# Optimization experiments

Hardware: AMD Instinct MI355X
Metric: run time of the kernel (lower is better)

## Reference

```python
import jax, jax.numpy as jnp
import numpy as np

EPS = 1e-8

def rms_norm(x, scale):
    # norm(2,-1)/sqrt(d); x / (rms + eps) * scale
    d = x.shape[-1]
    norm = jnp.sqrt(jnp.sum(x * x, axis=-1, keepdims=True))
    rms = norm / jnp.sqrt(jnp.asarray(d, x.dtype))
    return scale * (x / (rms + EPS))

def setup_inputs() -> dict:
    key = jax.random.key(0)
    B, N, C, FF = 2, 2048, 1024, 4096
    ks = jax.random.split(key, 12)
    s = 0.02
    return {
        "x":  jax.random.normal(ks[0], (B, N, C), jnp.float32),
        "wq": jax.random.normal(ks[1], (C, C), jnp.float32) * s,
        "bq": jnp.zeros((C,), jnp.float32),
        "wk": jax.random.normal(ks[2], (C, C), jnp.float32) * s,
        "bk": jnp.zeros((C,), jnp.float32),
        "wv": jax.random.normal(ks[3], (C, C), jnp.float32) * s,
        "bv": jnp.zeros((C,), jnp.float32),
        "wo": jax.random.normal(ks[4], (C, C), jnp.float32) * s,
        "bo": jnp.zeros((C,), jnp.float32),
        "scale1": jnp.ones((C,), jnp.float32),
        "scale2": jnp.ones((C,), jnp.float32),
        "w1": jax.random.normal(ks[5], (C, FF), jnp.float32) * s,
        "b1": jnp.zeros((FF,), jnp.float32),
        "w2": jax.random.normal(ks[6], (FF, C), jnp.float32) * s,
        "b2": jnp.zeros((C,), jnp.float32),
    }

def reference(x, wq, bq, wk, bk, wv, bv, wo, bo, scale1, scale2, w1, b1, w2, b2):
    B, N, C = x.shape
    H = 16
    D = C // H

    residual = x
    xn = rms_norm(x, scale1)

    def heads(y):  # [B,N,C] -> [B,H,N,D]
        return y.reshape(B, N, H, D).transpose(0, 2, 1, 3)

    q = heads(xn @ wq + bq)
    k = heads(xn @ wk + bk)
    v = heads(xn @ wv + bv)

    # apply_rotary_pos_emb with cos=sin=1: q' = q - roll(q,1,-1), same for k
    q = q - jnp.roll(q, 1, axis=-1)
    k = k - jnp.roll(k, 1, axis=-1)

    # explicit attention (no causal mask in original)
    scores = jnp.einsum('bhnd,bhmd->bhnm', q, k) / jnp.sqrt(jnp.asarray(D, x.dtype))
    probs = jax.nn.softmax(scores, axis=-1)
    attn = jnp.einsum('bhnm,bhmd->bhnd', probs, v)
    attn = attn.transpose(0, 2, 1, 3).reshape(B, N, C)
    attn = attn @ wo + bo

    x = residual + attn
    residual = x
    xn = rms_norm(x, scale2)
    h = jax.nn.gelu(xn @ w1 + b1, approximate=False)  # torch GELU default = exact
    ffn_out = h @ w2 + b2
    return residual + ffn_out
```

## Files before the change

kernel.cpp:

```cpp
#include <hip/hip_runtime.h>
#include <hip/hip_bf16.h>
#include <math.h>

typedef unsigned short u16;
typedef short s16x8 __attribute__((ext_vector_type(8)));
typedef short s16x4 __attribute__((ext_vector_type(4)));
typedef __bf16 bf16x8v __attribute__((ext_vector_type(8)));
typedef float f32x4 __attribute__((ext_vector_type(4)));
typedef unsigned short u16x4 __attribute__((ext_vector_type(4)));

struct Ptr4 { float* p[4]; };
struct TW6 {
    const float* w[6]; u16* o[6]; int mode[6];
    const float *bq, *bk, *bv; float* bqkv;
};

__device__ __forceinline__ u16 f2b(float f) {
    __hip_bfloat16 h = __float2bfloat16(f);
    return __builtin_bit_cast(u16, h);
}

__device__ __forceinline__ float exp2_fast(float x) {
#if __has_builtin(__builtin_amdgcn_exp2f)
    return __builtin_amdgcn_exp2f(x);
#else
    return exp2f(x);
#endif
}

__device__ __forceinline__ f32x4 mfma16(s16x8 a, s16x8 b, f32x4 c) {
    return __builtin_amdgcn_mfma_f32_16x16x32_bf16(
        __builtin_bit_cast(bf16x8v, a), __builtin_bit_cast(bf16x8v, b), c, 0, 0, 0);
}

__device__ __forceinline__ void gl_lds16(const void* g, void* l) {
    typedef const unsigned int __attribute__((address_space(1))) * gp_t;
    typedef unsigned int __attribute__((address_space(3))) * lp_t;
    __builtin_amdgcn_global_load_lds((gp_t)(unsigned long long)g,
                                     (lp_t)(unsigned int)(unsigned long long)l,
                                     16, 0, 0);
}

__device__ __forceinline__ float gelu_fast(float v) {
    float u = 1.5957691216f * (v + 0.044715f * v * v * v);
    return v / (1.f + __expf(-u));
}

#define QSCALE 0.1803368801111244f

__global__ __launch_bounds__(256) void prep_weights(TW6 io) {
    const int z = blockIdx.z, bx = blockIdx.x, by = blockIdx.y;
    const float* W; u16* Wt; int mode = 0, N_, K_, n0, k0;
    if (z < 4) {
        if (bx >= 32) {
            if (z == 0 && bx < 44 && by == 0) {
                const int i = (bx - 32) * 256 + threadIdx.x;
                const int d = i & 1023;
                const int dp = (d & ~63) | ((d + 63) & 63);
                float v;
                if (i < 1024) v = QSCALE * (io.bq[d] - io.bq[dp]);
                else if (i < 2048) v = io.bk[d] - io.bk[dp];
                else v = io.bv[d];
                io.bqkv[i] = v;
            }
            return;
        }
        W = io.w[z]; Wt = io.o[z]; mode = io.mode[z];
        N_ = 1024; K_ = 1024; n0 = bx * 32; k0 = by * 32;
    } else if (z == 4) {
        W = io.w[4]; Wt = io.o[4]; N_ = 4096; K_ = 1024; n0 = bx * 32; k0 = by * 32;
    } else {
        W = io.w[5]; Wt = io.o[5]; N_ = 1024; K_ = 4096; n0 = by * 32; k0 = bx * 32;
    }
    __shared__ u16 tile[32][33];
    const int tx = threadIdx.x & 31, ty = threadIdx.x >> 5;
    const int n = n0 + tx;
    const int np = (n & ~63) | ((n + 63) & 63);
    const float s = (mode == 1) ? QSCALE : 1.f;
#pragma unroll
    for (int i = 0; i < 32; i += 8) {
        const size_t r = (size_t)(k0 + ty + i) * N_;
        float v = W[r + n];
        if (mode) v = (v - W[r + np]) * s;
        tile[ty + i][tx] = f2b(v);
    }
    __syncthreads();
#pragma unroll
    for (int i = 0; i < 32; i += 8)
        Wt[(size_t)(n0 + ty + i) * K_ + k0 + tx] = tile[tx][ty + i];
}

__global__ __launch_bounds__(256) void transpose_v(const u16* __restrict__ qkv,
                                                   u16* __restrict__ vT) {
    __shared__ u16 tile[32][33];
    const int tx = threadIdx.x & 31, ty = threadIdx.x >> 5;
    const int n0 = blockIdx.x * 32, d0 = blockIdx.y * 32, bh = blockIdx.z;
    const int b = bh >> 4, h = bh & 15;
#pragma unroll
    for (int i = 0; i < 32; i += 8)
        tile[ty + i][tx] =
            qkv[(size_t)(b * 2048 + n0 + ty + i) * 3072 + 2048 + h * 64 + d0 + tx];
    __syncthreads();
#pragma unroll
    for (int i = 0; i < 32; i += 8)
        vT[((size_t)bh * 64 + d0 + ty + i) * 2048 + n0 + tx] = tile[tx][ty + i];
}

__global__ __launch_bounds__(256) void rmsnorm_kernel(const float* __restrict__ x,
                                                      const float* __restrict__ scale,
                                                      u16* __restrict__ out) {
    __shared__ float red[4];
    const int t = threadIdx.x, row = blockIdx.x;
    const float4* xr = (const float4*)(x + (size_t)row * 1024);
    float4 v = xr[t];
    float ss = v.x * v.x + v.y * v.y + v.z * v.z + v.w * v.w;
#pragma unroll
    for (int off = 1; off < 64; off <<= 1) ss += __shfl_xor(ss, off);
    if ((t & 63) == 0) red[t >> 6] = ss;
    __syncthreads();
    float tot = red[0] + red[1] + red[2] + red[3];
    float inv = 1.f / (sqrtf(tot * (1.f / 1024.f)) + 1e-8f);
    const float4* sr = (const float4*)scale;
    float4 s = sr[t];
    u16x4 o;
    o[0] = f2b(v.x * inv * s.x);
    o[1] = f2b(v.y * inv * s.y);
    o[2] = f2b(v.z * inv * s.z);
    o[3] = f2b(v.w * inv * s.w);
    ((u16x4*)(out + (size_t)row * 1024))[t] = o;
}

template <int EPI>
__global__ __launch_bounds__(512, 2) void gemm256(const u16* __restrict__ A,
                                                  const u16* __restrict__ Bt,
                                                  const float* __restrict__ bias,
                                                  Ptr4 parts,
                                                  u16* __restrict__ outp,
                                                  int Nout, int nTN, int cpx,
                                                  int Ktot) {
    __shared__ __align__(16) u16 sm[65536];
    u16* As = sm;
    u16* Bs = sm + 32768;

    const int t = threadIdx.x, lane = t & 63, w = t >> 6;
    const int c = lane & 15, qd = lane >> 4;
    const int wm = (w >> 2) * 128, wn = (w & 3) * 64;

    const int id = (int)blockIdx.x;
    const int l = (id & 7) * cpx + (id >> 3);
    const int m0 = (l / nTN) * 256, n0 = (l % nTN) * 256;
    const int k0 = (EPI == 3) ? (int)blockIdx.y * 1024 : 0;
    float* pout = (EPI == 3) ? parts.p[blockIdx.y] : nullptr;

    const int srow = t >> 3;
    const int sch8 = ((t & 7) ^ (srow & 7)) * 8;
    const u16* Ag = A + (size_t)(m0 + srow) * Ktot + k0 + sch8;
    const u16* Bg = Bt + (size_t)(n0 + srow) * Ktot + k0 + sch8;

    float bv[4];
    if (EPI != 3) {
#pragma unroll
        for (int n = 0; n < 4; ++n) bv[n] = bias[n0 + wn + n * 16 + c];
        asm volatile("" ::: "memory");
    }

    auto stageA = [&](int kt, int h, int s) {
        const u16* src = Ag + (size_t)(h * 128) * Ktot + kt * 64;
        u16* dst = As + s * 16384 + h * 8192 + t * 8;
        gl_lds16(src, dst);
        gl_lds16(src + (size_t)64 * Ktot, dst + 4096);
    };
    auto stageB = [&](int kt, int h, int s) {
        const u16* src = Bg + (size_t)(h * 128) * Ktot + kt * 64;
        u16* dst = Bs + s * 16384 + h * 8192 + t * 8;
        gl_lds16(src, dst);
        gl_lds16(src + (size_t)64 * Ktot, dst + 4096);
    };

    stageA(0, 0, 0); stageA(0, 1, 0);
    stageB(0, 0, 0); stageB(0, 1, 0);
    stageB(1, 0, 1); stageB(1, 1, 1);
    asm volatile("s_waitcnt vmcnt(4)" ::: "memory");
    __builtin_amdgcn_s_barrier();
    __builtin_amdgcn_sched_barrier(0);

    f32x4 acc[8][4] = {};

    for (int it = 0; it < 8; ++it) {
        const int ktA = 2 * it, ktB = 2 * it + 1;
        s16x8 bf[4][2];

#pragma unroll
        for (int q = 0; q < 4; ++q) {
            s16x8 af[2][2];
            if (q == 0) {
#pragma unroll
                for (int n = 0; n < 4; ++n)
#pragma unroll
                    for (int ks = 0; ks < 2; ++ks)
                        bf[n][ks] = *(const s16x8*)&Bs[(wn + n * 16 + c) * 64 +
                                                       (((ks * 4 + qd) ^ (c & 7)) * 8)];
            }
#pragma unroll
            for (int mm = 0; mm < 2; ++mm)
#pragma unroll
                for (int ks = 0; ks < 2; ++ks)
                    af[mm][ks] = *(const s16x8*)&As[(wm + (2 * q + mm) * 16 + c) * 64 +
                                                    (((ks * 4 + qd) ^ (c & 7)) * 8)];
            if (q == 0) {
                stageA(ktB, 0, 1);
            } else if (q == 1) {
                stageA(ktB, 1, 1);
                if (ktA + 2 < 16) stageB(ktA + 2, 0, 0);
            } else if (q == 2) {
                if (ktA + 2 < 16) stageB(ktA + 2, 1, 0);
            }
            __builtin_amdgcn_s_barrier();
            asm volatile("s_waitcnt lgkmcnt(0)" ::: "memory");
            __builtin_amdgcn_sched_barrier(0);
            __builtin_amdgcn_s_setprio(1);
#pragma unroll
            for (int mm = 0; mm < 2; ++mm)
#pragma unroll
                for (int n = 0; n < 4; ++n)
#pragma unroll
                    for (int ks = 0; ks < 2; ++ks)
                        acc[2 * q + mm][n] =
                            mfma16(af[mm][ks], bf[n][ks], acc[2 * q + mm][n]);
            __builtin_amdgcn_s_setprio(0);
            if (q == 3) {
                if (it < 7)
                    asm volatile("s_waitcnt vmcnt(4)" ::: "memory");
                else
                    asm volatile("s_waitcnt vmcnt(0)" ::: "memory");
            }
            __builtin_amdgcn_s_barrier();
        }

#pragma unroll
        for (int q = 0; q < 4; ++q) {
            s16x8 af[2][2];
            if (q == 0) {
#pragma unroll
                for (int n = 0; n < 4; ++n)
#pragma unroll
                    for (int ks = 0; ks < 2; ++ks)
                        bf[n][ks] = *(const s16x8*)&Bs[16384 + (wn + n * 16 + c) * 64 +
                                                       (((ks * 4 + qd) ^ (c & 7)) * 8)];
            }
#pragma unroll
            for (int mm = 0; mm < 2; ++mm)
#pragma unroll
                for (int ks = 0; ks < 2; ++ks)
                    af[mm][ks] = *(const s16x8*)&As[16384 + (wm + (2 * q + mm) * 16 + c) * 64 +
                                                    (((ks * 4 + qd) ^ (c & 7)) * 8)];
            if (q == 0) {
                if (ktA + 2 < 16) stageA(ktA + 2, 0, 0);
            } else if (q == 1) {
                if (ktA + 2 < 16) stageA(ktA + 2, 1, 0);
            } else if (q == 2) {
                if (ktB + 2 < 16) stageB(ktB + 2, 0, 1);
            } else {
                if (ktB + 2 < 16) stageB(ktB + 2, 1, 1);
            }
            __builtin_amdgcn_s_barrier();
            asm volatile("s_waitcnt lgkmcnt(0)" ::: "memory");
            __builtin_amdgcn_sched_barrier(0);
            __builtin_amdgcn_s_setprio(1);
#pragma unroll
            for (int mm = 0; mm < 2; ++mm)
#pragma unroll
                for (int n = 0; n < 4; ++n)
#pragma unroll
                    for (int ks = 0; ks < 2; ++ks)
                        acc[2 * q + mm][n] =
                            mfma16(af[mm][ks], bf[n][ks], acc[2 * q + mm][n]);
            __builtin_amdgcn_s_setprio(0);
            if (q == 3 && it < 7)
                asm volatile("s_waitcnt vmcnt(4)" ::: "memory");
            __builtin_amdgcn_s_barrier();
        }
    }

#pragma unroll
    for (int m = 0; m < 8; ++m)
#pragma unroll
        for (int n = 0; n < 4; ++n) {
            const int colg = n0 + wn + n * 16 + c;
#pragma unroll
            for (int r = 0; r < 4; ++r) {
                const int rowg = m0 + wm + m * 16 + qd * 4 + r;
                if (EPI == 0) {
                    outp[(size_t)rowg * Nout + colg] = f2b(acc[m][n][r] + bv[n]);
                } else if (EPI == 2) {
                    outp[(size_t)rowg * Nout + colg] =
                        f2b(gelu_fast(acc[m][n][r] + bv[n]));
                } else {
                    pout[(size_t)rowg * 1024 + colg] = acc[m][n][r];
                }
            }
        }
}

__global__ __launch_bounds__(256) void gemm_splitk(const u16* __restrict__ A,
                                                   const u16* __restrict__ Bt,
                                                   Ptr4 parts,
                                                   int N, int Ktot, int Kc) {
    __shared__ __align__(16) u16 As[128 * 64];
    __shared__ __align__(16) u16 Bs[128 * 64];
    const int t = threadIdx.x, lane = t & 63;
    const int w = t >> 6, wm = (w >> 1) * 64, wn = (w & 1) * 64;
    const int c = lane & 15, qd = lane >> 4;
    const int n0 = blockIdx.x * 128, m0 = blockIdx.y * 128;
    const int z = blockIdx.z;
    float* out = parts.p[z];

    const int srow = t >> 3;
    const int sch8 = ((t & 7) ^ (srow & 7)) * 8;
    const u16* Ag = A + (size_t)(m0 + srow) * Ktot + z * Kc + sch8;
    const u16* Bg = Bt + (size_t)(n0 + srow) * Ktot + z * Kc + sch8;
    const size_t rstride = (size_t)32 * Ktot;

    f32x4 acc[4][4] = {};
    for (int kt = 0; kt < Kc; kt += 64) {
        __syncthreads();
#pragma unroll
        for (int g = 0; g < 4; g++) {
            gl_lds16(Ag + g * rstride, &As[t * 8 + g * 2048]);
            gl_lds16(Bg + g * rstride, &Bs[t * 8 + g * 2048]);
        }
        Ag += 64;
        Bg += 64;
        __syncthreads();
#pragma unroll
        for (int s = 0; s < 2; s++) {
            s16x8 a[4], b[4];
#pragma unroll
            for (int im = 0; im < 4; im++)
                a[im] = *(const s16x8*)&As[(wm + im * 16 + c) * 64 +
                                           (((s * 4 + qd) ^ (c & 7)) * 8)];
#pragma unroll
            for (int jn = 0; jn < 4; jn++)
                b[jn] = *(const s16x8*)&Bs[(wn + jn * 16 + c) * 64 +
                                           (((s * 4 + qd) ^ (c & 7)) * 8)];
#pragma unroll
            for (int im = 0; im < 4; im++)
#pragma unroll
                for (int jn = 0; jn < 4; jn++)
                    acc[im][jn] = mfma16(a[im], b[jn], acc[im][jn]);
        }
    }

#pragma unroll
    for (int im = 0; im < 4; im++)
#pragma unroll
        for (int jn = 0; jn < 4; jn++) {
            const int colg = n0 + wn + jn * 16 + c;
#pragma unroll
            for (int r = 0; r < 4; r++) {
                const int rowg = m0 + wm + im * 16 + qd * 4 + r;
                out[(size_t)rowg * N + colg] = acc[im][jn][r];
            }
        }
}

template <int S, bool NORM>
__global__ __launch_bounds__(256) void reduce_kernel(Ptr4 parts,
                                                     const float* __restrict__ bias,
                                                     const float* __restrict__ resid,
                                                     const float* __restrict__ scale,
                                                     float* __restrict__ yout,
                                                     u16* __restrict__ xnout) {
    __shared__ float red[4];
    const int t = threadIdx.x, row = blockIdx.x;
    const size_t base = (size_t)row * 1024;
    float4 v = ((const float4*)(resid + base))[t];
    float4 bv = ((const float4*)bias)[t];
    v.x += bv.x; v.y += bv.y; v.z += bv.z; v.w += bv.w;
#pragma unroll
    for (int s = 0; s < S; s++) {
        float4 pv = ((const float4*)(parts.p[s] + base))[t];
        v.x += pv.x; v.y += pv.y; v.z += pv.z; v.w += pv.w;
    }
    ((float4*)(yout + base))[t] = v;
    if (NORM) {
        float ss = v.x * v.x + v.y * v.y + v.z * v.z + v.w * v.w;
#pragma unroll
        for (int off = 1; off < 64; off <<= 1) ss += __shfl_xor(ss, off);
        if ((t & 63) == 0) red[t >> 6] = ss;
        __syncthreads();
        float tot = red[0] + red[1] + red[2] + red[3];
        float inv = 1.f / (sqrtf(tot * (1.f / 1024.f)) + 1e-8f);
        float4 s = ((const float4*)scale)[t];
        u16x4 o;
        o[0] = f2b(v.x * inv * s.x);
        o[1] = f2b(v.y * inv * s.y);
        o[2] = f2b(v.z * inv * s.z);
        o[3] = f2b(v.w * inv * s.w);
        ((u16x4*)(xnout + base))[t] = o;
    }
}

__global__ __launch_bounds__(256, 2) void attn_kernel(const u16* __restrict__ qkv,
                                                      const u16* __restrict__ vT,
                                                      u16* __restrict__ attn) {
    __shared__ __align__(16) char smem[65536];
    __shared__ float LS[4][64];
    u16* SM = (u16*)smem;

    const int t = threadIdx.x, lane = t & 63, w = t >> 6;
    const int c = lane & 15, g = lane >> 4;

    const int id = blockIdx.x;
    const int logical = (id & 7) * 128 + (id >> 3);
    const int bh = logical >> 5, qb = logical & 31;
    const int b = bh >> 4, h = bh & 15;
    const int q0 = qb * 64;
    const size_t rowbase = (size_t)b * 2048;

    const u16* kg = qkv + rowbase * 3072 + 1024 + h * 64;
    const u16* vg = vT + (size_t)bh * 64 * 2048;

    u16* WS = SM + w * 8192;

    const int kr = lane >> 3, ks8 = lane & 7;
    const int ksw = (ks8 ^ (kr & 7)) * 8;
    const int vr = lane >> 1, vh = (lane & 1) * 8;

    auto stage = [&](int it, int bi) {
        u16* B = WS + bi * 2048;
        const u16* kq = kg + (size_t)(it * 64 + w * 16) * 3072;
        const u16* vq = vg + it * 64 + w * 16;
        gl_lds16(kq + (size_t)kr * 3072 + ksw,       &B[lane * 8]);
        gl_lds16(kq + (size_t)(kr + 8) * 3072 + ksw, &B[512 + lane * 8]);
        gl_lds16(vq + (size_t)vr * 2048 + vh,        &B[1024 + lane * 8]);
        gl_lds16(vq + (size_t)(vr + 32) * 2048 + vh, &B[1536 + lane * 8]);
    };

    s16x8 qf[4][2];
    {
        const u16* qg = qkv + (rowbase + q0) * 3072 + h * 64;
#pragma unroll
        for (int jn = 0; jn < 4; jn++)
#pragma unroll
            for (int ks = 0; ks < 2; ks++)
                qf[jn][ks] = *(const s16x8*)&qg[(size_t)(jn * 16 + c) * 3072 +
                                                ks * 32 + g * 8];
    }

    stage(0, 0);
    stage(1, 1);
    stage(2, 2);
    stage(3, 3);

    f32x4 acc[4][4] = {};
    float ls[4] = {};

    for (int j = 0; j < 16; j++) {
        if (j < 15)
            asm volatile("s_waitcnt vmcnt(8)" ::: "memory");
        else
            asm volatile("s_waitcnt vmcnt(0)" ::: "memory");
        __builtin_amdgcn_sched_barrier(0);

        const u16* Kb0 = WS + ((2 * j) & 3) * 2048;
        const u16* Kb1 = WS + ((2 * j + 1) & 3) * 2048;
        const u16* Vb0 = Kb0 + 1024;
        const u16* Vb1 = Kb1 + 1024;

        s16x8 kf0[2], kf1[2];
#pragma unroll
        for (int ks = 0; ks < 2; ks++) {
            const int sw = ((ks * 4 + g) ^ (c & 7)) * 8;
            kf0[ks] = *(const s16x8*)&Kb0[c * 64 + sw];
            kf1[ks] = *(const s16x8*)&Kb1[c * 64 + sw];
        }
        s16x8 vf[4];
#pragma unroll
        for (int im = 0; im < 4; im++) {
            s16x4 v0 = *(const s16x4*)&Vb0[(im * 16 + c) * 16 + g * 4];
            s16x4 v1 = *(const s16x4*)&Vb1[(im * 16 + c) * 16 + g * 4];
            vf[im] = __builtin_shufflevector(v0, v1, 0, 1, 2, 3, 4, 5, 6, 7);
        }

        s16x8 pb[4];
        {
            f32x4 sc[4] = {};
            __builtin_amdgcn_s_setprio(1);
#pragma unroll
            for (int ks = 0; ks < 2; ks++)
#pragma unroll
                for (int jn = 0; jn < 4; jn++)
                    sc[jn] = mfma16(kf0[ks], qf[jn][ks], sc[jn]);
            __builtin_amdgcn_s_setprio(0);
#pragma unroll
            for (int jn = 0; jn < 4; jn++) {
                float p0 = exp2_fast(sc[jn][0]);
                float p1 = exp2_fast(sc[jn][1]);
                float p2 = exp2_fast(sc[jn][2]);
                float p3 = exp2_fast(sc[jn][3]);
                ls[jn] += (p0 + p1) + (p2 + p3);
                pb[jn][0] = f2b(p0); pb[jn][1] = f2b(p1);
                pb[jn][2] = f2b(p2); pb[jn][3] = f2b(p3);
            }
        }
        {
            f32x4 sc[4] = {};
            __builtin_amdgcn_s_setprio(1);
#pragma unroll
            for (int ks = 0; ks < 2; ks++)
#pragma unroll
                for (int jn = 0; jn < 4; jn++)
                    sc[jn] = mfma16(kf1[ks], qf[jn][ks], sc[jn]);
            __builtin_amdgcn_s_setprio(0);
#pragma unroll
            for (int jn = 0; jn < 4; jn++) {
                float p0 = exp2_fast(sc[jn][0]);
                float p1 = exp2_fast(sc[jn][1]);
                float p2 = exp2_fast(sc[jn][2]);
                float p3 = exp2_fast(sc[jn][3]);
                ls[jn] += (p0 + p1) + (p2 + p3);
                pb[jn][4] = f2b(p0); pb[jn][5] = f2b(p1);
                pb[jn][6] = f2b(p2); pb[jn][7] = f2b(p3);
            }
        }

        __builtin_amdgcn_s_setprio(1);
#pragma unroll
        for (int im = 0; im < 4; im++)
#pragma unroll
            for (int jn = 0; jn < 4; jn++)
                acc[im][jn] = mfma16(vf[im], pb[jn], acc[im][jn]);
        __builtin_amdgcn_s_setprio(0);

        __builtin_amdgcn_sched_barrier(0);
        if (j < 14) {
            stage(2 * j + 4, (2 * j) & 3);
            stage(2 * j + 5, (2 * j + 1) & 3);
        }
    }

#pragma unroll
    for (int jn = 0; jn < 4; jn++) {
        float v = ls[jn];
        v += __shfl_xor(v, 16);
        v += __shfl_xor(v, 32);
        ls[jn] = v;
    }
    if (lane < 16) {
#pragma unroll
        for (int jn = 0; jn < 4; jn++) LS[w][jn * 16 + lane] = ls[jn];
    }

    float* SC = (float*)smem;
#pragma unroll
    for (int src = 3; src >= 1; --src) {
        __syncthreads();
        if (w == src) {
#pragma unroll
            for (int im = 0; im < 4; im++)
#pragma unroll
                for (int jn = 0; jn < 4; jn++)
#pragma unroll
                    for (int r = 0; r < 4; r++)
                        SC[(im * 16 + g * 4 + r) * 66 + jn * 16 + c] =
                            acc[im][jn][r];
        }
        __syncthreads();
        if (w == src - 1) {
#pragma unroll
            for (int im = 0; im < 4; im++)
#pragma unroll
                for (int jn = 0; jn < 4; jn++)
#pragma unroll
                    for (int r = 0; r < 4; r++)
                        acc[im][jn][r] +=
                            SC[(im * 16 + g * 4 + r) * 66 + jn * 16 + c];
        }
    }
    __syncthreads();

    u16* OT = (u16*)smem;
    if (w == 0) {
#pragma unroll
        for (int jn = 0; jn < 4; jn++) {
            const int q = jn * 16 + c;
            const float inv = 1.f / (LS[0][q] + LS[1][q] + LS[2][q] + LS[3][q]);
#pragma unroll
            for (int im = 0; im < 4; im++)
#pragma unroll
                for (int r = 0; r < 4; r++)
                    OT[q * 72 + im * 16 + g * 4 + r] = f2b(acc[im][jn][r] * inv);
        }
    }
    __syncthreads();

    {
        const int q = t >> 2, d0 = (t & 3) * 16;
        const int grow = b * 2048 + q0 + q;
        u16* dst = attn + (size_t)grow * 1024 + h * 64 + d0;
        *(s16x8*)dst = *(const s16x8*)&OT[q * 72 + d0];
        *((s16x8*)dst + 1) = *((const s16x8*)&OT[q * 72 + d0] + 1);
    }
}

extern "C" void kernel_launch(void* const* d_in, const int* in_sizes, int n_in,
                              void* d_out, int out_size, void* d_ws, size_t ws_size,
                              hipStream_t stream) {
    const float* x = (const float*)d_in[0];
    const float* wq = (const float*)d_in[1];
    const float* bq = (const float*)d_in[2];
    const float* wk = (const float*)d_in[3];
    const float* bk = (const float*)d_in[4];
    const float* wv = (const float*)d_in[5];
    const float* bv = (const float*)d_in[6];
    const float* wo = (const float*)d_in[7];
    const float* bo = (const float*)d_in[8];
    const float* scale1 = (const float*)d_in[9];
    const float* scale2 = (const float*)d_in[10];
    const float* w1 = (const float*)d_in[11];
    const float* b1 = (const float*)d_in[12];
    const float* w2 = (const float*)d_in[13];
    const float* b2 = (const float*)d_in[14];
    float* out = (float*)d_out;

    char* ws = (char*)d_ws;
    size_t off = 0;
    auto alloc = [&](size_t bytes) -> char* {
        char* p = ws + off;
        off += (bytes + 255) & ~(size_t)255;
        return p;
    };
    u16* wqkvT = (u16*)alloc((size_t)3072 * 1024 * 2);
    u16* woT   = (u16*)alloc((size_t)1024 * 1024 * 2);
    u16* w1T   = (u16*)alloc((size_t)4096 * 1024 * 2);
    u16* w2T   = (u16*)alloc((size_t)1024 * 4096 * 2);
    float* bqkv = (float*)alloc(3072 * 4);
    u16* xn    = (u16*)alloc((size_t)4096 * 1024 * 2);
    u16* qkv   = (u16*)alloc((size_t)4096 * 3072 * 2);
    u16* vT    = (u16*)alloc((size_t)32 * 64 * 2048 * 2);
    u16* attnb = (u16*)alloc((size_t)4096 * 1024 * 2);
    float* y1  = (float*)alloc((size_t)4096 * 1024 * 4);
    u16* hbuf  = (u16*)alloc((size_t)4096 * 4096 * 2);

    const size_t SPLIT = (size_t)4096 * 1024;
    Ptr4 po; po.p[0] = (float*)qkv; po.p[1] = (float*)qkv + SPLIT;
    po.p[2] = nullptr; po.p[3] = nullptr;
    Ptr4 pf; pf.p[0] = (float*)xn; pf.p[1] = (float*)xn + SPLIT;
    pf.p[2] = (float*)xn + 2 * SPLIT; pf.p[3] = (float*)wqkvT;
    Ptr4 pz = {};

    dim3 blk(256);

    TW6 tw;
    tw.w[0] = wq; tw.o[0] = wqkvT;                          tw.mode[0] = 1;
    tw.w[1] = wk; tw.o[1] = wqkvT + (size_t)1024 * 1024;    tw.mode[1] = 2;
    tw.w[2] = wv; tw.o[2] = wqkvT + (size_t)2048 * 1024;    tw.mode[2] = 0;
    tw.w[3] = wo; tw.o[3] = woT;                            tw.mode[3] = 0;
    tw.w[4] = w1; tw.o[4] = w1T;                            tw.mode[4] = 0;
    tw.w[5] = w2; tw.o[5] = w2T;                            tw.mode[5] = 0;
    tw.bq = bq; tw.bk = bk; tw.bv = bv; tw.bqkv = bqkv;
    prep_weights<<<dim3(128, 32, 6), blk, 0, stream>>>(tw);

    rmsnorm_kernel<<<4096, blk, 0, stream>>>(x, scale1, xn);
    gemm256<0><<<dim3(192), dim3(512), 0, stream>>>(xn, wqkvT, bqkv, pz, qkv, 3072, 12, 24, 1024);
    transpose_v<<<dim3(64, 2, 32), blk, 0, stream>>>(qkv, vT);
    attn_kernel<<<dim3(1024), blk, 0, stream>>>(qkv, vT, attnb);
    gemm_splitk<<<dim3(8, 32, 2), blk, 0, stream>>>(attnb, woT, po, 1024, 1024, 512);
    reduce_kernel<2, true><<<4096, blk, 0, stream>>>(po, bo, x, scale2, y1, xn);
    gemm256<2><<<dim3(256), dim3(512), 0, stream>>>(xn, w1T, b1, pz, hbuf, 4096, 16, 32, 1024);
    gemm256<3><<<dim3(64, 4), dim3(512), 0, stream>>>(hbuf, w2T, nullptr, pf, nullptr, 1024, 4, 8, 4096);
    reduce_kernel<4, false><<<4096, blk, 0, stream>>>(pf, b2, y1, nullptr, out, nullptr);
}
```

Before: 341.9 us.

## Fuse first rmsnorm into weight prep and replace FFN split-K reduce with atomics

The first RMSNorm now runs as an extra z-slice of the weight-preparation launch, removing a separate kernel launch. The attention-output reduce kernel now also writes the residual plus b2 directly into the output buffer as a seed. The FFN down-projection split-K GEMM then accumulates its partials into that buffer with atomicAdd, eliminating the final reduce kernel, the y1 buffer and the partial-sum writes and reads. In exchange it adds atomic contention and makes the summation order nondeterministic.

```diff
diff --git a/kernel.cpp b/kernel.cpp
--- a/kernel.cpp
+++ b/kernel.cpp
@@ -13,6 +13,7 @@
 struct TW6 {
     const float* w[6]; u16* o[6]; int mode[6];
     const float *bq, *bk, *bv; float* bqkv;
+    const float *x, *s1; u16* xn;
 };
 
 __device__ __forceinline__ u16 f2b(float f) {
@@ -50,6 +51,30 @@
 
 __global__ __launch_bounds__(256) void prep_weights(TW6 io) {
     const int z = blockIdx.z, bx = blockIdx.x, by = blockIdx.y;
+    __shared__ u16 tile[32][33];
+    __shared__ float red[4];
+
+    if (z == 6) {
+        const int t = threadIdx.x, row = by * 128 + bx;
+        const float4* xr = (const float4*)(io.x + (size_t)row * 1024);
+        float4 v = xr[t];
+        float ss = v.x * v.x + v.y * v.y + v.z * v.z + v.w * v.w;
+#pragma unroll
+        for (int off = 1; off < 64; off <<= 1) ss += __shfl_xor(ss, off);
+        if ((t & 63) == 0) red[t >> 6] = ss;
+        __syncthreads();
+        float tot = red[0] + red[1] + red[2] + red[3];
+        float inv = 1.f / (sqrtf(tot * (1.f / 1024.f)) + 1e-8f);
+        float4 s = ((const float4*)io.s1)[t];
+        u16x4 o;
+        o[0] = f2b(v.x * inv * s.x);
+        o[1] = f2b(v.y * inv * s.y);
+        o[2] = f2b(v.z * inv * s.z);
+        o[3] = f2b(v.w * inv * s.w);
+        ((u16x4*)(io.xn + (size_t)row * 1024))[t] = o;
+        return;
+    }
+
     const float* W; u16* Wt; int mode = 0, N_, K_, n0, k0;
     if (z < 4) {
         if (bx >= 32) {
@@ -72,7 +97,6 @@
     } else {
         W = io.w[5]; Wt = io.o[5]; N_ = 1024; K_ = 4096; n0 = by * 32; k0 = bx * 32;
     }
-    __shared__ u16 tile[32][33];
     const int tx = threadIdx.x & 31, ty = threadIdx.x >> 5;
     const int n = n0 + tx;
     const int np = (n & ~63) | ((n + 63) & 63);
@@ -106,35 +130,11 @@
         vT[((size_t)bh * 64 + d0 + ty + i) * 2048 + n0 + tx] = tile[tx][ty + i];
 }
 
-__global__ __launch_bounds__(256) void rmsnorm_kernel(const float* __restrict__ x,
-                                                      const float* __restrict__ scale,
-                                                      u16* __restrict__ out) {
-    __shared__ float red[4];
-    const int t = threadIdx.x, row = blockIdx.x;
-    const float4* xr = (const float4*)(x + (size_t)row * 1024);
-    float4 v = xr[t];
-    float ss = v.x * v.x + v.y * v.y + v.z * v.z + v.w * v.w;
-#pragma unroll
-    for (int off = 1; off < 64; off <<= 1) ss += __shfl_xor(ss, off);
-    if ((t & 63) == 0) red[t >> 6] = ss;
-    __syncthreads();
-    float tot = red[0] + red[1] + red[2] + red[3];
-    float inv = 1.f / (sqrtf(tot * (1.f / 1024.f)) + 1e-8f);
-    const float4* sr = (const float4*)scale;
-    float4 s = sr[t];
-    u16x4 o;
-    o[0] = f2b(v.x * inv * s.x);
-    o[1] = f2b(v.y * inv * s.y);
-    o[2] = f2b(v.z * inv * s.z);
-    o[3] = f2b(v.w * inv * s.w);
-    ((u16x4*)(out + (size_t)row * 1024))[t] = o;
-}
-
 template <int EPI>
 __global__ __launch_bounds__(512, 2) void gemm256(const u16* __restrict__ A,
                                                   const u16* __restrict__ Bt,
                                                   const float* __restrict__ bias,
-                                                  Ptr4 parts,
+                                                  float* __restrict__ outf,
                                                   u16* __restrict__ outp,
                                                   int Nout, int nTN, int cpx,
                                                   int Ktot) {
@@ -150,7 +150,6 @@
     const int l = (id & 7) * cpx + (id >> 3);
     const int m0 = (l / nTN) * 256, n0 = (l % nTN) * 256;
     const int k0 = (EPI == 3) ? (int)blockIdx.y * 1024 : 0;
-    float* pout = (EPI == 3) ? parts.p[blockIdx.y] : nullptr;
 
     const int srow = t >> 3;
     const int sch8 = ((t & 7) ^ (srow & 7)) * 8;
@@ -296,7 +295,7 @@
                     outp[(size_t)rowg * Nout + colg] =
                         f2b(gelu_fast(acc[m][n][r] + bv[n]));
                 } else {
-                    pout[(size_t)rowg * 1024 + colg] = acc[m][n][r];
+                    atomicAdd(outf + (size_t)rowg * 1024 + colg, acc[m][n][r]);
                 }
             }
         }
@@ -364,41 +363,44 @@
         }
 }
 
-template <int S, bool NORM>
-__global__ __launch_bounds__(256) void reduce_kernel(Ptr4 parts,
-                                                     const float* __restrict__ bias,
-                                                     const float* __restrict__ resid,
-                                                     const float* __restrict__ scale,
-                                                     float* __restrict__ yout,
-                                                     u16* __restrict__ xnout) {
+__global__ __launch_bounds__(256) void reduce_norm_seed(Ptr4 parts,
+                                                        const float* __restrict__ bo_,
+                                                        const float* __restrict__ resid,
+                                                        const float* __restrict__ scale,
+                                                        const float* __restrict__ b2_,
+                                                        float* __restrict__ outseed,
+                                                        u16* __restrict__ xnout) {
     __shared__ float red[4];
     const int t = threadIdx.x, row = blockIdx.x;
     const size_t base = (size_t)row * 1024;
     float4 v = ((const float4*)(resid + base))[t];
-    float4 bv = ((const float4*)bias)[t];
+    float4 bv = ((const float4*)bo_)[t];
     v.x += bv.x; v.y += bv.y; v.z += bv.z; v.w += bv.w;
 #pragma unroll
-    for (int s = 0; s < S; s++) {
+    for (int s = 0; s < 2; s++) {
         float4 pv = ((const float4*)(parts.p[s] + base))[t];
         v.x += pv.x; v.y += pv.y; v.z += pv.z; v.w += pv.w;
     }
-    ((float4*)(yout + base))[t] = v;
-    if (NORM) {
-        float ss = v.x * v.x + v.y * v.y + v.z * v.z + v.w * v.w;
-#pragma unroll
-        for (int off = 1; off < 64; off <<= 1) ss += __shfl_xor(ss, off);
-        if ((t & 63) == 0) red[t >> 6] = ss;
-        __syncthreads();
-        float tot = red[0] + red[1] + red[2] + red[3];
-        float inv = 1.f / (sqrtf(tot * (1.f / 1024.f)) + 1e-8f);
-        float4 s = ((const float4*)scale)[t];
-        u16x4 o;
-        o[0] = f2b(v.x * inv * s.x);
-        o[1] = f2b(v.y * inv * s.y);
-        o[2] = f2b(v.z * inv * s.z);
-        o[3] = f2b(v.w * inv * s.w);
-        ((u16x4*)(xnout + base))[t] = o;
-    }
+    float4 b2v = ((const float4*)b2_)[t];
+    float4 sd;
+    sd.x = v.x + b2v.x; sd.y = v.y + b2v.y;
+    sd.z = v.z + b2v.z; sd.w = v.w + b2v.w;
+    ((float4*)(outseed + base))[t] = sd;
+
+    float ss = v.x * v.x + v.y * v.y + v.z * v.z + v.w * v.w;
+#pragma unroll
+    for (int off = 1; off < 64; off <<= 1) ss += __shfl_xor(ss, off);
+    if ((t & 63) == 0) red[t >> 6] = ss;
+    __syncthreads();
+    float tot = red[0] + red[1] + red[2] + red[3];
+    float inv = 1.f / (sqrtf(tot * (1.f / 1024.f)) + 1e-8f);
+    float4 s = ((const float4*)scale)[t];
+    u16x4 o;
+    o[0] = f2b(v.x * inv * s.x);
+    o[1] = f2b(v.y * inv * s.y);
+    o[2] = f2b(v.z * inv * s.z);
+    o[3] = f2b(v.w * inv * s.w);
+    ((u16x4*)(xnout + base))[t] = o;
 }
 
 __global__ __launch_bounds__(256, 2) void attn_kernel(const u16* __restrict__ qkv,
@@ -640,15 +642,11 @@
     u16* qkv   = (u16*)alloc((size_t)4096 * 3072 * 2);
     u16* vT    = (u16*)alloc((size_t)32 * 64 * 2048 * 2);
     u16* attnb = (u16*)alloc((size_t)4096 * 1024 * 2);
-    float* y1  = (float*)alloc((size_t)4096 * 1024 * 4);
     u16* hbuf  = (u16*)alloc((size_t)4096 * 4096 * 2);
 
     const size_t SPLIT = (size_t)4096 * 1024;
     Ptr4 po; po.p[0] = (float*)qkv; po.p[1] = (float*)qkv + SPLIT;
     po.p[2] = nullptr; po.p[3] = nullptr;
-    Ptr4 pf; pf.p[0] = (float*)xn; pf.p[1] = (float*)xn + SPLIT;
-    pf.p[2] = (float*)xn + 2 * SPLIT; pf.p[3] = (float*)wqkvT;
-    Ptr4 pz = {};
 
     dim3 blk(256);
 
@@ -660,15 +658,14 @@
     tw.w[4] = w1; tw.o[4] = w1T;                            tw.mode[4] = 0;
     tw.w[5] = w2; tw.o[5] = w2T;                            tw.mode[5] = 0;
     tw.bq = bq; tw.bk = bk; tw.bv = bv; tw.bqkv = bqkv;
-    prep_weights<<<dim3(128, 32, 6), blk, 0, stream>>>(tw);
-
-    rmsnorm_kernel<<<4096, blk, 0, stream>>>(x, scale1, xn);
-    gemm256<0><<<dim3(192), dim3(512), 0, stream>>>(xn, wqkvT, bqkv, pz, qkv, 3072, 12, 24, 1024);
+    tw.x = x; tw.s1 = scale1; tw.xn = xn;
+
+    prep_weights<<<dim3(128, 32, 7), blk, 0, stream>>>(tw);
+    gemm256<0><<<dim3(192), dim3(512), 0, stream>>>(xn, wqkvT, bqkv, nullptr, qkv, 3072, 12, 24, 1024);
     transpose_v<<<dim3(64, 2, 32), blk, 0, stream>>>(qkv, vT);
     attn_kernel<<<dim3(1024), blk, 0, stream>>>(qkv, vT, attnb);
     gemm_splitk<<<dim3(8, 32, 2), blk, 0, stream>>>(attnb, woT, po, 1024, 1024, 512);
-    reduce_kernel<2, true><<<4096, blk, 0, stream>>>(po, bo, x, scale2, y1, xn);
-    gemm256<2><<<dim3(256), dim3(512), 0, stream>>>(xn, w1T, b1, pz, hbuf, 4096, 16, 32, 1024);
-    gemm256<3><<<dim3(64, 4), dim3(512), 0, stream>>>(hbuf, w2T, nullptr, pf, nullptr, 1024, 4, 8, 4096);
-    reduce_kernel<4, false><<<4096, blk, 0, stream>>>(pf, b2, y1, nullptr, out, nullptr);
-}
+    reduce_norm_seed<<<4096, blk, 0, stream>>>(po, bo, x, scale2, b2, out, xn);
+    gemm256<2><<<dim3(256), dim3(512), 0, stream>>>(xn, w1T, b1, nullptr, hbuf, 4096, 16, 32, 1024);
+    gemm256<3><<<dim3(64, 4), dim3(512), 0, stream>>>(hbuf, w2T, nullptr, out, nullptr, 1024, 4, 8, 4096);
+}
```

Result: slower. 367.6 us (+7.5%).
